# Kernel tuning notes

Measured on AMD Instinct MI355X. Metric: run time of the kernel, lower is better.

Reference implementation:

```python
import jax, jax.numpy as jnp
import numpy as np

VOCAB, EMBED, H = 32000, 128, 128
B, T = 32, 2048


def setup_inputs() -> dict:
    key = jax.random.key(0)
    ks = jax.random.split(key, 8)
    tokens = jax.random.randint(ks[0], (B, T), 0, VOCAB, dtype=jnp.int32)
    emb = jax.random.normal(ks[1], (VOCAB, EMBED), jnp.float32) * 0.05
    # layer 0: input EMBED -> H ; layer 1: H -> H
    Wx0 = jax.random.normal(ks[2], (EMBED, H), jnp.float32) * (1.0 / np.sqrt(EMBED))
    Wh0 = jax.random.normal(ks[3], (H, H), jnp.float32) * (1.0 / np.sqrt(H))
    b0 = jnp.zeros((H,), jnp.float32)
    Wx1 = jax.random.normal(ks[4], (H, H), jnp.float32) * (1.0 / np.sqrt(H))
    Wh1 = jax.random.normal(ks[5], (H, H), jnp.float32) * (1.0 / np.sqrt(H))
    b1 = jnp.zeros((H,), jnp.float32)
    return {"tokens": tokens, "emb": emb, "Wx0": Wx0, "Wh0": Wh0, "b0": b0,
            "Wx1": Wx1, "Wh1": Wh1, "b1": b1}


def _simple_rnn(x, mask, Wx, Wh, b):
    # x: [B,T,Din], mask: [B,T] bool. Keras masked-step semantics: at masked
    # steps, state (== output for SimpleRNN) carries over unchanged.
    xt = jnp.swapaxes(x, 0, 1)                 # [T,B,Din]
    xproj = xt @ Wx + b                        # precompute input projection [T,B,H]
    mt = jnp.swapaxes(mask, 0, 1)[..., None]   # [T,B,1]
    h0 = jnp.zeros((x.shape[0], Wh.shape[0]), x.dtype)

    def step(h, inp):
        xp, m = inp
        h_new = jnp.tanh(xp + h @ Wh)
        h = jnp.where(m, h_new, h)
        return h, h

    _, ys = jax.lax.scan(step, h0, (xproj, mt))
    return jnp.swapaxes(ys, 0, 1)              # [B,T,H]


def reference(tokens, emb, Wx0, Wh0, b0, Wx1, Wh1, b1):
    mask = tokens != 0                          # mask_zero=True
    x = emb[tokens]                             # [B,T,E]
    x = _simple_rnn(x, mask, Wx0, Wh0, b0)
    x = _simple_rnn(x, mask, Wx1, Wh1, b1)
    return x
```

## Files before the change

kernel.cpp:

```cpp
#include <hip/hip_runtime.h>
#include <math.h>

#define BB 32
#define TT 2048
#define HH 128

#define LDS_BARRIER() asm volatile("s_waitcnt lgkmcnt(0)\n\ts_barrier" ::: "memory")

#define QPERM_F(v, CTRL)                                                      \
  __int_as_float(__builtin_amdgcn_update_dpp(                                 \
      0, __float_as_int(v), (CTRL), 0xF, 0xF, true))

template <bool GATHER>
__global__ __launch_bounds__(256) void proj_kernel(
    const float* __restrict__ src, const int* __restrict__ tokens,
    const float* __restrict__ W, const float* __restrict__ bias,
    float* __restrict__ out) {
  const int tid = threadIdx.x;
  const int jj = tid & 31;
  const int rr = tid >> 5;
  const int base = blockIdx.x * 64;

  __shared__ __align__(16) float srow[64][HH];
  __shared__ int stok[64];

  if (GATHER) {
    if (tid < 64) stok[tid] = tokens[base + tid];
    __syncthreads();
  }

#pragma unroll
  for (int i = 0; i < 8; ++i) {
    int idx = tid + i * 256;
    int row = idx >> 5;
    int c4 = idx & 31;
    const float* s = GATHER ? (src + (size_t)stok[row] * HH)
                            : (src + (size_t)(base + row) * HH);
    *(float4*)&srow[row][c4 * 4] = *(const float4*)&s[c4 * 4];
  }
  __syncthreads();

  float4 b4 = *(const float4*)&bias[jj * 4];
  float4 acc[8];
#pragma unroll
  for (int i = 0; i < 8; ++i) acc[i] = b4;

  for (int k = 0; k < HH; ++k) {
    float4 w4 = *(const float4*)&W[k * HH + jj * 4];
#pragma unroll
    for (int i = 0; i < 8; ++i) {
      float e = srow[rr * 8 + i][k];
      acc[i].x += e * w4.x;
      acc[i].y += e * w4.y;
      acc[i].z += e * w4.z;
      acc[i].w += e * w4.w;
    }
  }

#pragma unroll
  for (int i = 0; i < 8; ++i) {
    int row = base + rr * 8 + i;
    *(float4*)&out[(size_t)row * HH + jj * 4] = acc[i];
  }
}

__global__ __launch_bounds__(512) void rnn_kernel(
    float* io, const float* __restrict__ Wh, const int* __restrict__ tokens) {
  const int b = blockIdx.x;
  const int tid = threadIdx.x;
  const int j = tid >> 2;
  const int p = tid & 3;
  const int lane = tid & 63;

  float w[32];
#pragma unroll
  for (int c = 0; c < 32; ++c) {
    int k = 16 * (c >> 2) + 4 * p + (c & 3);
    w[c] = Wh[k * HH + j];
  }

  const int* tok = tokens + b * TT;
  unsigned bits = 0;
#pragma unroll
  for (int i = 0; i < 8; ++i) {
    int4 tk = *(const int4*)&tok[lane * 32 + i * 4];
    bits |= (unsigned)(tk.x != 0) << (i * 4 + 0);
    bits |= (unsigned)(tk.y != 0) << (i * 4 + 1);
    bits |= (unsigned)(tk.z != 0) << (i * 4 + 2);
    bits |= (unsigned)(tk.w != 0) << (i * 4 + 3);
  }

  __shared__ __align__(16) float hs[2][HH];
  if (tid < HH) hs[0][tid] = 0.0f;

  float* xp = io + (size_t)b * TT * HH;

  float h = 0.0f;
  float xcur = xp[(size_t)p * HH + j];
  LDS_BARRIER();

#define RNN_STEP(Q)                                                           \
  {                                                                           \
    const int t = t0 + (Q);                                                   \
    const float* hb = hs[t & 1];                                              \
    float a0 = 0.f, a1 = 0.f, a2 = 0.f, a3 = 0.f;                             \
    _Pragma("unroll") for (int i = 0; i < 8; ++i) {                           \
      float4 hv = *(const float4*)&hb[16 * i + 4 * p];                        \
      a0 += hv.x * w[4 * i + 0];                                              \
      a1 += hv.y * w[4 * i + 1];                                              \
      a2 += hv.z * w[4 * i + 2];                                              \
      a3 += hv.w * w[4 * i + 3];                                              \
    }                                                                         \
    float acc = (a0 + a1) + (a2 + a3);                                        \
    acc += QPERM_F(acc, 0xB1);                                     \
    acc += QPERM_F(acc, 0x4E);                                     \
    float x = QPERM_F(xcur, (Q)*0x55);             \
    float s = acc + x;                                                        \
    unsigned word =                                                           \
        (unsigned)__builtin_amdgcn_readlane((int)bits, t >> 5);               \
    int m = (word >> (t & 31)) & 1;                                           \
    float ax = fabsf(s);                                                      \
    float e = __expf(-2.0f * ax);                                             \
    float th = (1.0f - e) * __builtin_amdgcn_rcpf(1.0f + e);                  \
    th = copysignf(th, s);                                                    \
    h = m ? th : h;                                                           \
    if (p == 0) {                                                             \
      xp[(size_t)t * HH + j] = h;                   \
      hs[(t + 1) & 1][j] = h;                                  \
    }                                                                         \
    LDS_BARRIER();                                                            \
  }

  for (int t0 = 0; t0 < TT; t0 += 4) {
    float xnext = 0.0f;
    if (t0 + 4 < TT) xnext = xp[(size_t)(t0 + 4 + p) * HH + j];
    RNN_STEP(0)
    RNN_STEP(1)
    RNN_STEP(2)
    RNN_STEP(3)
    xcur = xnext;
  }
#undef RNN_STEP
}

extern "C" void kernel_launch(void* const* d_in, const int* in_sizes, int n_in,
                              void* d_out, int out_size, void* d_ws,
                              size_t ws_size, hipStream_t stream) {
  const int* tokens = (const int*)d_in[0];
  const float* emb = (const float*)d_in[1];
  const float* Wx0 = (const float*)d_in[2];
  const float* Wh0 = (const float*)d_in[3];
  const float* b0 = (const float*)d_in[4];
  const float* Wx1 = (const float*)d_in[5];
  const float* Wh1 = (const float*)d_in[6];
  const float* b1 = (const float*)d_in[7];
  float* out = (float*)d_out;
  float* ws = (float*)d_ws;

  const int rows = BB * TT;
  const int proj_blocks = rows / 64;

  proj_kernel<true><<<proj_blocks, 256, 0, stream>>>(emb, tokens, Wx0, b0, ws);
  rnn_kernel<<<BB, 512, 0, stream>>>(ws, Wh0, tokens);
  proj_kernel<false><<<proj_blocks, 256, 0, stream>>>(ws, nullptr, Wx1, b1, out);
  rnn_kernel<<<BB, 512, 0, stream>>>(out, Wh1, tokens);
}
```

Baseline: 1.406 ms.

## Fuse both RNN layers into one wavefront-pipelined kernel

Runs the two RNN layers in a single 1024-thread block per batch row. Threads 0-511 run layer 0 and threads 512-1023 run layer 1 one step behind, reading layer 0's hidden state straight from shared memory. The layer-1 input projection is folded into the recurrence, which removes the second projection kernel, one launch and an HBM round trip of the intermediate sequence. In exchange each layer-1 step does twice the dot-product work, the two layers share barriers in lockstep, and the doubled thread count raises register pressure.

```diff
diff --git a/kernel.cpp b/kernel.cpp
--- a/kernel.cpp
+++ b/kernel.cpp
@@ -11,7 +11,6 @@
   __int_as_float(__builtin_amdgcn_update_dpp(                                 \
       0, __float_as_int(v), (CTRL), 0xF, 0xF, true))
 
-template <bool GATHER>
 __global__ __launch_bounds__(256) void proj_kernel(
     const float* __restrict__ src, const int* __restrict__ tokens,
     const float* __restrict__ W, const float* __restrict__ bias,
@@ -24,18 +23,15 @@
   __shared__ __align__(16) float srow[64][HH];
   __shared__ int stok[64];
 
-  if (GATHER) {
-    if (tid < 64) stok[tid] = tokens[base + tid];
-    __syncthreads();
-  }
+  if (tid < 64) stok[tid] = tokens[base + tid];
+  __syncthreads();
 
 #pragma unroll
   for (int i = 0; i < 8; ++i) {
     int idx = tid + i * 256;
     int row = idx >> 5;
     int c4 = idx & 31;
-    const float* s = GATHER ? (src + (size_t)stok[row] * HH)
-                            : (src + (size_t)(base + row) * HH);
+    const float* s = src + (size_t)stok[row] * HH;
     *(float4*)&srow[row][c4 * 4] = *(const float4*)&s[c4 * 4];
   }
   __syncthreads();
@@ -64,20 +60,18 @@
   }
 }
 
-__global__ __launch_bounds__(512) void rnn_kernel(
-    float* io, const float* __restrict__ Wh, const int* __restrict__ tokens) {
+__global__ __launch_bounds__(1024) void rnn_fused(
+    const float* __restrict__ xp0, float* __restrict__ out,
+    const float* __restrict__ Wh0, const float* __restrict__ Wx1,
+    const float* __restrict__ Wh1, const float* __restrict__ b1,
+    const int* __restrict__ tokens) {
   const int b = blockIdx.x;
   const int tid = threadIdx.x;
-  const int j = tid >> 2;
-  const int p = tid & 3;
+  const bool isL0 = (tid < 512);
+  const int sub = tid & 511;
+  const int j = sub >> 2;
+  const int p = sub & 3;
   const int lane = tid & 63;
-
-  float w[32];
-#pragma unroll
-  for (int c = 0; c < 32; ++c) {
-    int k = 16 * (c >> 2) + 4 * p + (c & 3);
-    w[c] = Wh[k * HH + j];
-  }
 
   const int* tok = tokens + b * TT;
   unsigned bits = 0;
@@ -90,57 +84,123 @@
     bits |= (unsigned)(tk.w != 0) << (i * 4 + 3);
   }
 
-  __shared__ __align__(16) float hs[2][HH];
-  if (tid < HH) hs[0][tid] = 0.0f;
-
-  float* xp = io + (size_t)b * TT * HH;
-
-  float h = 0.0f;
-  float xcur = xp[(size_t)p * HH + j];
+  __shared__ __align__(16) float hs0[2][HH];
+  __shared__ __align__(16) float hs1[2][HH];
+  if (tid < HH) {
+    hs0[0][tid] = 0.0f;
+    hs0[1][tid] = 0.0f;
+    hs1[0][tid] = 0.0f;
+    hs1[1][tid] = 0.0f;
+  }
   LDS_BARRIER();
 
-#define RNN_STEP(Q)                                                           \
+  if (isL0) {
+    float w0[32];
+#pragma unroll
+    for (int c = 0; c < 32; ++c) {
+      int k = 16 * (c >> 2) + 4 * p + (c & 3);
+      w0[c] = Wh0[k * HH + j];
+    }
+    const float* xb = xp0 + (size_t)b * TT * HH;
+    float h0 = 0.0f;
+    float xc = xb[(size_t)p * HH + j];
+
+#define L0_STEP(Q)                                                            \
   {                                                                           \
     const int t = t0 + (Q);                                                   \
-    const float* hb = hs[t & 1];                                              \
+    const float* hb = hs0[(Q) & 1];                                           \
     float a0 = 0.f, a1 = 0.f, a2 = 0.f, a3 = 0.f;                             \
     _Pragma("unroll") for (int i = 0; i < 8; ++i) {                           \
       float4 hv = *(const float4*)&hb[16 * i + 4 * p];                        \
-      a0 += hv.x * w[4 * i + 0];                                              \
-      a1 += hv.y * w[4 * i + 1];                                              \
-      a2 += hv.z * w[4 * i + 2];                                              \
-      a3 += hv.w * w[4 * i + 3];                                              \
+      a0 += hv.x * w0[4 * i + 0];                                             \
+      a1 += hv.y * w0[4 * i + 1];                                             \
+      a2 += hv.z * w0[4 * i + 2];                                             \
+      a3 += hv.w * w0[4 * i + 3];                                             \
     }                                                                         \
     float acc = (a0 + a1) + (a2 + a3);                                        \
-    acc += QPERM_F(acc, 0xB1);                                     \
-    acc += QPERM_F(acc, 0x4E);                                     \
-    float x = QPERM_F(xcur, (Q)*0x55);             \
-    float s = acc + x;                                                        \
-    unsigned word =                                                           \
-        (unsigned)__builtin_amdgcn_readlane((int)bits, t >> 5);               \
+    acc += QPERM_F(acc, 0xB1);                                                \
+    acc += QPERM_F(acc, 0x4E);                                                \
+    float sx = acc + QPERM_F(xc, (Q) * 0x55);                                 \
+    unsigned word = (unsigned)__builtin_amdgcn_readlane((int)bits, t >> 5);   \
     int m = (word >> (t & 31)) & 1;                                           \
-    float ax = fabsf(s);                                                      \
-    float e = __expf(-2.0f * ax);                                             \
-    float th = (1.0f - e) * __builtin_amdgcn_rcpf(1.0f + e);                  \
-    th = copysignf(th, s);                                                    \
-    h = m ? th : h;                                                           \
+    float e = __expf(-2.0f * fabsf(sx));                                      \
+    float th = copysignf((1.0f - e) * __builtin_amdgcn_rcpf(1.0f + e), sx);   \
+    h0 = m ? th : h0;                                                         \
+    if (p == 0) hs0[((Q) + 1) & 1][j] = h0;                                   \
+    LDS_BARRIER();                                                            \
+  }
+
+    for (int t0 = 0; t0 < TT; t0 += 4) {
+      float xn = 0.0f;
+      if (t0 + 4 < TT) xn = xb[(size_t)(t0 + 4 + p) * HH + j];
+      L0_STEP(0)
+      L0_STEP(1)
+      L0_STEP(2)
+      L0_STEP(3)
+      xc = xn;
+    }
+#undef L0_STEP
+  } else {
+    float wx[32], wh[32];
+#pragma unroll
+    for (int c = 0; c < 32; ++c) {
+      int k = 16 * (c >> 2) + 4 * p + (c & 3);
+      wx[c] = Wx1[k * HH + j];
+      wh[c] = Wh1[k * HH + j];
+    }
+    const float bias1 = b1[j];
+    float* ob = out + (size_t)b * TT * HH;
+    float h1 = 0.0f;
+
+#define L1_BODY(PH, PAR)                                                      \
+  {                                                                           \
+    const int t = (PH)-1;                                                     \
+    const float* yb = hs0[(PAR)];                                             \
+    const float* hb = hs1[(PAR)];                                             \
+    float a0 = 0.f, a1 = 0.f, a2 = 0.f, a3 = 0.f;                             \
+    float c0 = 0.f, c1 = 0.f, c2 = 0.f, c3 = 0.f;                             \
+    _Pragma("unroll") for (int i = 0; i < 8; ++i) {                           \
+      float4 yv = *(const float4*)&yb[16 * i + 4 * p];                        \
+      float4 hv = *(const float4*)&hb[16 * i + 4 * p];                        \
+      a0 += yv.x * wx[4 * i + 0];                                             \
+      a1 += yv.y * wx[4 * i + 1];                                             \
+      a2 += yv.z * wx[4 * i + 2];                                             \
+      a3 += yv.w * wx[4 * i + 3];                                             \
+      c0 += hv.x * wh[4 * i + 0];                                             \
+      c1 += hv.y * wh[4 * i + 1];                                             \
+      c2 += hv.z * wh[4 * i + 2];                                             \
+      c3 += hv.w * wh[4 * i + 3];                                             \
+    }                                                                         \
+    float acc = ((a0 + a1) + (a2 + a3)) + ((c0 + c1) + (c2 + c3));            \
+    acc += QPERM_F(acc, 0xB1);                                                \
+    acc += QPERM_F(acc, 0x4E);                                                \
+    float sx = acc + bias1;                                                   \
+    unsigned word = (unsigned)__builtin_amdgcn_readlane((int)bits, t >> 5);   \
+    int m = (word >> (t & 31)) & 1;                                           \
+    float e = __expf(-2.0f * fabsf(sx));                                      \
+    float th = copysignf((1.0f - e) * __builtin_amdgcn_rcpf(1.0f + e), sx);   \
+    h1 = m ? th : h1;                                                         \
     if (p == 0) {                                                             \
-      xp[(size_t)t * HH + j] = h;                   \
-      hs[(t + 1) & 1][j] = h;                                  \
+      ob[(size_t)t * HH + j] = h1;                                            \
+      hs1[(PAR) ^ 1][j] = h1;                                                 \
     }                                                                         \
-    LDS_BARRIER();                                                            \
-  }
-
-  for (int t0 = 0; t0 < TT; t0 += 4) {
-    float xnext = 0.0f;
-    if (t0 + 4 < TT) xnext = xp[(size_t)(t0 + 4 + p) * HH + j];
-    RNN_STEP(0)
-    RNN_STEP(1)
-    RNN_STEP(2)
-    RNN_STEP(3)
-    xcur = xnext;
-  }
-#undef RNN_STEP
+  }
+
+    for (int ph0 = 0; ph0 < TT; ph0 += 4) {
+      if (ph0 > 0) {
+        L1_BODY(ph0 + 0, 0)
+      }
+      LDS_BARRIER();
+      L1_BODY(ph0 + 1, 1)
+      LDS_BARRIER();
+      L1_BODY(ph0 + 2, 0)
+      LDS_BARRIER();
+      L1_BODY(ph0 + 3, 1)
+      LDS_BARRIER();
+    }
+    L1_BODY(TT, 0)
+#undef L1_BODY
+  }
 }
 
 extern "C" void kernel_launch(void* const* d_in, const int* in_sizes, int n_in,
@@ -160,8 +220,6 @@
   const int rows = BB * TT;
   const int proj_blocks = rows / 64;
 
-  proj_kernel<true><<<proj_blocks, 256, 0, stream>>>(emb, tokens, Wx0, b0, ws);
-  rnn_kernel<<<BB, 512, 0, stream>>>(ws, Wh0, tokens);
-  proj_kernel<false><<<proj_blocks, 256, 0, stream>>>(ws, nullptr, Wx1, b1, out);
-  rnn_kernel<<<BB, 512, 0, stream>>>(out, Wh1, tokens);
+  proj_kernel<<<proj_blocks, 256, 0, stream>>>(emb, tokens, Wx0, b0, ws);
+  rnn_fused<<<BB, 1024, 0, stream>>>(ws, out, Wh0, Wx1, Wh1, b1, tokens);
 }
```

Measured after the change: 4.575 ms. +225.3%, slower.

## Remap RNN recurrence to 8 lanes per two output columns

Applied to the files above, without the earlier changes.

Reorganizes the recurrent matvec so each group of 8 lanes computes two hidden columns (cp and cp+64), each lane covering 16 k-values per column, with a three-stage DPP reduction within the 8-lane group. The input projection values are now loaded per lane into registers for four steps rather than broadcast via DPP. The goal is to halve the LDS reads of h per column and shorten the per-step dependency chain, at the cost of an extra DPP reduction stage, more per-lane global loads and two writer lanes per group.

```diff
diff --git a/kernel.cpp b/kernel.cpp
--- a/kernel.cpp
+++ b/kernel.cpp
@@ -7,7 +7,7 @@
 
 #define LDS_BARRIER() asm volatile("s_waitcnt lgkmcnt(0)\n\ts_barrier" ::: "memory")
 
-#define QPERM_F(v, CTRL)                                                      \
+#define DPP_F(v, CTRL)                                                        \
   __int_as_float(__builtin_amdgcn_update_dpp(                                 \
       0, __float_as_int(v), (CTRL), 0xF, 0xF, true))
 
@@ -68,15 +68,17 @@
     float* io, const float* __restrict__ Wh, const int* __restrict__ tokens) {
   const int b = blockIdx.x;
   const int tid = threadIdx.x;
-  const int j = tid >> 2;
-  const int p = tid & 3;
+  const int cp = tid >> 3;
+  const int p = tid & 7;
   const int lane = tid & 63;
+  const int colsel = cp + ((p & 1) << 6);
 
-  float w[32];
+  float w0[16], w1[16];
 #pragma unroll
-  for (int c = 0; c < 32; ++c) {
-    int k = 16 * (c >> 2) + 4 * p + (c & 3);
-    w[c] = Wh[k * HH + j];
+  for (int c = 0; c < 16; ++c) {
+    int k = 32 * (c >> 2) + 4 * p + (c & 3);
+    w0[c] = Wh[k * HH + cp];
+    w1[c] = Wh[k * HH + cp + 64];
   }
 
   const int* tok = tokens + b * TT;
@@ -95,50 +97,68 @@
 
   float* xp = io + (size_t)b * TT * HH;
 
+  float xr[4];
+#pragma unroll
+  for (int i = 0; i < 4; ++i) xr[i] = xp[(size_t)i * HH + colsel];
+
   float h = 0.0f;
-  float xcur = xp[(size_t)p * HH + j];
   LDS_BARRIER();
 
 #define RNN_STEP(Q)                                                           \
   {                                                                           \
     const int t = t0 + (Q);                                                   \
-    const float* hb = hs[t & 1];                                              \
+    const float* hb = hs[(Q) & 1];                                            \
     float a0 = 0.f, a1 = 0.f, a2 = 0.f, a3 = 0.f;                             \
-    _Pragma("unroll") for (int i = 0; i < 8; ++i) {                           \
-      float4 hv = *(const float4*)&hb[16 * i + 4 * p];                        \
-      a0 += hv.x * w[4 * i + 0];                                              \
-      a1 += hv.y * w[4 * i + 1];                                              \
-      a2 += hv.z * w[4 * i + 2];                                              \
-      a3 += hv.w * w[4 * i + 3];                                              \
+    float c0 = 0.f, c1 = 0.f, c2 = 0.f, c3 = 0.f;                             \
+    _Pragma("unroll") for (int i = 0; i < 4; ++i) {                           \
+      float4 hv = *(const float4*)&hb[32 * i + 4 * p];                        \
+      a0 += hv.x * w0[4 * i + 0];                                             \
+      a1 += hv.y * w0[4 * i + 1];                                             \
+      a2 += hv.z * w0[4 * i + 2];                                             \
+      a3 += hv.w * w0[4 * i + 3];                                             \
+      c0 += hv.x * w1[4 * i + 0];                                             \
+      c1 += hv.y * w1[4 * i + 1];                                             \
+      c2 += hv.z * w1[4 * i + 2];                                             \
+      c3 += hv.w * w1[4 * i + 3];                                             \
     }                                                                         \
-    float acc = (a0 + a1) + (a2 + a3);                                        \
-    acc += QPERM_F(acc, 0xB1);                                     \
-    acc += QPERM_F(acc, 0x4E);                                     \
-    float x = QPERM_F(xcur, (Q)*0x55);             \
-    float s = acc + x;                                                        \
-    unsigned word =                                                           \
-        (unsigned)__builtin_amdgcn_readlane((int)bits, t >> 5);               \
+    float accA = (a0 + a1) + (a2 + a3);                                       \
+    float accB = (c0 + c1) + (c2 + c3);                                       \
+    accA += DPP_F(accA, 0xB1);                           \
+    accB += DPP_F(accB, 0xB1);                                                \
+    accA += DPP_F(accA, 0x4E);                           \
+    accB += DPP_F(accB, 0x4E);                                                \
+    accA += DPP_F(accA, 0x141);                \
+    accB += DPP_F(accB, 0x141);                                               \
+    float acc = (p & 1) ? accB : accA;                                        \
+    float sx = acc + xr[(Q)];                                                 \
+    unsigned word = (unsigned)__builtin_amdgcn_readlane((int)bits, t >> 5);   \
     int m = (word >> (t & 31)) & 1;                                           \
-    float ax = fabsf(s);                                                      \
-    float e = __expf(-2.0f * ax);                                             \
-    float th = (1.0f - e) * __builtin_amdgcn_rcpf(1.0f + e);                  \
-    th = copysignf(th, s);                                                    \
+    float e = __expf(-2.0f * fabsf(sx));                                      \
+    float th = copysignf((1.0f - e) * __builtin_amdgcn_rcpf(1.0f + e), sx);   \
     h = m ? th : h;                                                           \
-    if (p == 0) {                                                             \
-      xp[(size_t)t * HH + j] = h;                   \
-      hs[(t + 1) & 1][j] = h;                                  \
+    if (p < 2) {                                                              \
+      xp[(size_t)t * HH + colsel] = h;              \
+      hs[((Q) + 1) & 1][colsel] = h;                           \
     }                                                                         \
     LDS_BARRIER();                                                            \
   }
 
   for (int t0 = 0; t0 < TT; t0 += 4) {
-    float xnext = 0.0f;
-    if (t0 + 4 < TT) xnext = xp[(size_t)(t0 + 4 + p) * HH + j];
+    float xn0 = 0.f, xn1 = 0.f, xn2 = 0.f, xn3 = 0.f;
+    if (t0 + 4 < TT) {
+      xn0 = xp[(size_t)(t0 + 4) * HH + colsel];
+      xn1 = xp[(size_t)(t0 + 5) * HH + colsel];
+      xn2 = xp[(size_t)(t0 + 6) * HH + colsel];
+      xn3 = xp[(size_t)(t0 + 7) * HH + colsel];
+    }
     RNN_STEP(0)
     RNN_STEP(1)
     RNN_STEP(2)
     RNN_STEP(3)
-    xcur = xnext;
+    xr[0] = xn0;
+    xr[1] = xn1;
+    xr[2] = xn2;
+    xr[3] = xn3;
   }
 #undef RNN_STEP
 }
```

Result: slower. 1.493 ms (+6.2%).

## Pipeline both RNN layers concurrently with chunked flag handoff and fused layer-1 projection

Applied to the files above, without the earlier changes.

Replaces the sequential layer-0 RNN, layer-1 projection and layer-1 RNN launches with one kernel of 64 blocks. The first 32 blocks run layer 0 and publish progress per 64-step chunk through global release flags. The other 32 run layer 1, spinning on those flags and computing the Wx1 input projection inline from a register ring buffer. This overlaps the two serial recurrences and removes the separate projection pass, at the cost of a doubled per-step dot product in layer 1 and cross-block spin-waiting that assumes all 64 blocks are co-resident. The old path remains as a fallback when the workspace is too small.

```diff
diff --git a/kernel.cpp b/kernel.cpp
--- a/kernel.cpp
+++ b/kernel.cpp
@@ -4,6 +4,9 @@
 #define BB 32
 #define TT 2048
 #define HH 128
+#define CHUNK 64
+#define NCH (TT / CHUNK)
+#define WS_HDR 4096
 
 #define LDS_BARRIER() asm volatile("s_waitcnt lgkmcnt(0)\n\ts_barrier" ::: "memory")
 
@@ -15,11 +18,14 @@
 __global__ __launch_bounds__(256) void proj_kernel(
     const float* __restrict__ src, const int* __restrict__ tokens,
     const float* __restrict__ W, const float* __restrict__ bias,
-    float* __restrict__ out) {
+    float* __restrict__ out, int* flags) {
   const int tid = threadIdx.x;
   const int jj = tid & 31;
   const int rr = tid >> 5;
   const int base = blockIdx.x * 64;
+
+  if (GATHER && flags != nullptr && blockIdx.x == 0 && tid < BB)
+    flags[tid] = 0;
 
   __shared__ __align__(16) float srow[64][HH];
   __shared__ int stok[64];
@@ -94,15 +100,14 @@
   if (tid < HH) hs[0][tid] = 0.0f;
 
   float* xp = io + (size_t)b * TT * HH;
-
   float h = 0.0f;
-  float xcur = xp[(size_t)p * HH + j];
+  float xc = xp[(size_t)p * HH + j];
   LDS_BARRIER();
 
 #define RNN_STEP(Q)                                                           \
   {                                                                           \
     const int t = t0 + (Q);                                                   \
-    const float* hb = hs[t & 1];                                              \
+    const float* hb = hs[(Q) & 1];                                            \
     float a0 = 0.f, a1 = 0.f, a2 = 0.f, a3 = 0.f;                             \
     _Pragma("unroll") for (int i = 0; i < 8; ++i) {                           \
       float4 hv = *(const float4*)&hb[16 * i + 4 * p];                        \
@@ -112,35 +117,191 @@
       a3 += hv.w * w[4 * i + 3];                                              \
     }                                                                         \
     float acc = (a0 + a1) + (a2 + a3);                                        \
-    acc += QPERM_F(acc, 0xB1);                                     \
-    acc += QPERM_F(acc, 0x4E);                                     \
-    float x = QPERM_F(xcur, (Q)*0x55);             \
-    float s = acc + x;                                                        \
-    unsigned word =                                                           \
-        (unsigned)__builtin_amdgcn_readlane((int)bits, t >> 5);               \
+    acc += QPERM_F(acc, 0xB1);                                                \
+    acc += QPERM_F(acc, 0x4E);                                                \
+    float sx = acc + QPERM_F(xc, (Q) * 0x55);                                 \
+    unsigned word = (unsigned)__builtin_amdgcn_readlane((int)bits, t >> 5);   \
     int m = (word >> (t & 31)) & 1;                                           \
-    float ax = fabsf(s);                                                      \
-    float e = __expf(-2.0f * ax);                                             \
-    float th = (1.0f - e) * __builtin_amdgcn_rcpf(1.0f + e);                  \
-    th = copysignf(th, s);                                                    \
+    float e = __expf(-2.0f * fabsf(sx));                                      \
+    float th = copysignf((1.0f - e) * __builtin_amdgcn_rcpf(1.0f + e), sx);   \
     h = m ? th : h;                                                           \
     if (p == 0) {                                                             \
-      xp[(size_t)t * HH + j] = h;                   \
-      hs[(t + 1) & 1][j] = h;                                  \
+      xp[(size_t)t * HH + j] = h;                                             \
+      hs[((Q) + 1) & 1][j] = h;                                               \
     }                                                                         \
     LDS_BARRIER();                                                            \
   }
 
   for (int t0 = 0; t0 < TT; t0 += 4) {
-    float xnext = 0.0f;
-    if (t0 + 4 < TT) xnext = xp[(size_t)(t0 + 4 + p) * HH + j];
+    float xn = 0.0f;
+    if (t0 + 4 < TT) xn = xp[(size_t)(t0 + 4 + p) * HH + j];
     RNN_STEP(0)
     RNN_STEP(1)
     RNN_STEP(2)
     RNN_STEP(3)
-    xcur = xnext;
+    xc = xn;
   }
 #undef RNN_STEP
+}
+
+__global__ __launch_bounds__(512) void rnn_pipe(
+    float* y0buf, float* __restrict__ out, const float* __restrict__ Wh0,
+    const float* __restrict__ Wx1, const float* __restrict__ Wh1,
+    const float* __restrict__ b1, const int* __restrict__ tokens,
+    int* flags) {
+  const int blk = blockIdx.x;
+  const bool isL0 = (blk < BB);
+  const int b = isL0 ? blk : blk - BB;
+  const int tid = threadIdx.x;
+  const int j = tid >> 2;
+  const int p = tid & 3;
+  const int lane = tid & 63;
+
+  const int* tok = tokens + b * TT;
+  unsigned bits = 0;
+#pragma unroll
+  for (int i = 0; i < 8; ++i) {
+    int4 tk = *(const int4*)&tok[lane * 32 + i * 4];
+    bits |= (unsigned)(tk.x != 0) << (i * 4 + 0);
+    bits |= (unsigned)(tk.y != 0) << (i * 4 + 1);
+    bits |= (unsigned)(tk.z != 0) << (i * 4 + 2);
+    bits |= (unsigned)(tk.w != 0) << (i * 4 + 3);
+  }
+
+  __shared__ __align__(16) float hs[2][HH];
+  if (tid < HH) hs[0][tid] = 0.0f;
+
+  float* y0 = y0buf + (size_t)b * TT * HH;
+
+  if (isL0) {
+    float w[32];
+#pragma unroll
+    for (int c = 0; c < 32; ++c) {
+      int k = 16 * (c >> 2) + 4 * p + (c & 3);
+      w[c] = Wh0[k * HH + j];
+    }
+    float h = 0.0f;
+    float xc = y0[(size_t)p * HH + j];
+    LDS_BARRIER();
+
+#define L0_STEP(Q)                                                            \
+  {                                                                           \
+    const int t = t0 + (Q);                                                   \
+    const float* hb = hs[(Q) & 1];                                            \
+    float a0 = 0.f, a1 = 0.f, a2 = 0.f, a3 = 0.f;                             \
+    _Pragma("unroll") for (int i = 0; i < 8; ++i) {                           \
+      float4 hv = *(const float4*)&hb[16 * i + 4 * p];                        \
+      a0 += hv.x * w[4 * i + 0];                                              \
+      a1 += hv.y * w[4 * i + 1];                                              \
+      a2 += hv.z * w[4 * i + 2];                                              \
+      a3 += hv.w * w[4 * i + 3];                                              \
+    }                                                                         \
+    float acc = (a0 + a1) + (a2 + a3);                                        \
+    acc += QPERM_F(acc, 0xB1);                                                \
+    acc += QPERM_F(acc, 0x4E);                                                \
+    float sx = acc + QPERM_F(xc, (Q) * 0x55);                                 \
+    unsigned word = (unsigned)__builtin_amdgcn_readlane((int)bits, t >> 5);   \
+    int m = (word >> (t & 31)) & 1;                                           \
+    float e = __expf(-2.0f * fabsf(sx));                                      \
+    float th = copysignf((1.0f - e) * __builtin_amdgcn_rcpf(1.0f + e), sx);   \
+    h = m ? th : h;                                                           \
+    if (p == 0) {                                                             \
+      y0[(size_t)t * HH + j] = h;                                             \
+      hs[((Q) + 1) & 1][j] = h;                                               \
+    }                                                                         \
+    LDS_BARRIER();                                                            \
+  }
+
+    for (int c = 0; c < NCH; ++c) {
+      for (int t0 = c * CHUNK; t0 < (c + 1) * CHUNK; t0 += 4) {
+        float xn = 0.0f;
+        if (t0 + 4 < TT) xn = y0[(size_t)(t0 + 4 + p) * HH + j];
+        L0_STEP(0)
+        L0_STEP(1)
+        L0_STEP(2)
+        L0_STEP(3)
+        xc = xn;
+      }
+      asm volatile("s_waitcnt vmcnt(0)" ::: "memory");
+      __syncthreads();
+      if (tid == 0) {
+        __threadfence();
+        __hip_atomic_store(&flags[b], c + 1, __ATOMIC_RELEASE,
+                           __HIP_MEMORY_SCOPE_AGENT);
+      }
+    }
+#undef L0_STEP
+  } else {
+    float wx[32], wh[32];
+#pragma unroll
+    for (int c = 0; c < 32; ++c) {
+      int k = 16 * (c >> 2) + 4 * p + (c & 3);
+      wx[c] = Wx1[k * HH + j];
+      wh[c] = Wh1[k * HH + j];
+    }
+    const float bias1 = b1[j];
+    float* ob = out + (size_t)b * TT * HH;
+    float h = 0.0f;
+    float4 ring0[8], ring1[8];
+    LDS_BARRIER();
+
+#define L1_STEP(Q, RG, RGN)                                                   \
+  {                                                                           \
+    const int t = t0 + (Q);                                                   \
+    const float* hb = hs[(Q) & 1];                                            \
+    float a0 = 0.f, a1 = 0.f, a2 = 0.f, a3 = 0.f;                             \
+    _Pragma("unroll") for (int i = 0; i < 8; ++i) {                           \
+      float4 hv = *(const float4*)&hb[16 * i + 4 * p];                        \
+      float4 yv = RG[i];                                                      \
+      a0 += hv.x * wh[4 * i + 0] + yv.x * wx[4 * i + 0];                      \
+      a1 += hv.y * wh[4 * i + 1] + yv.y * wx[4 * i + 1];                      \
+      a2 += hv.z * wh[4 * i + 2] + yv.z * wx[4 * i + 2];                      \
+      a3 += hv.w * wh[4 * i + 3] + yv.w * wx[4 * i + 3];                      \
+    }                                                                         \
+    if (t + 2 < TT) {                                                         \
+      const float* nsrc = y0 + (size_t)(t + 2) * HH + 4 * p;                  \
+      _Pragma("unroll") for (int i = 0; i < 8; ++i)                           \
+          RGN[i] = *(const float4*)(nsrc + 16 * i);                           \
+    }                                                                         \
+    float acc = (a0 + a1) + (a2 + a3);                                        \
+    acc += QPERM_F(acc, 0xB1);                                                \
+    acc += QPERM_F(acc, 0x4E);                                                \
+    float sx = acc + bias1;                                                   \
+    unsigned word = (unsigned)__builtin_amdgcn_readlane((int)bits, t >> 5);   \
+    int m = (word >> (t & 31)) & 1;                                           \
+    float e = __expf(-2.0f * fabsf(sx));                                      \
+    float th = copysignf((1.0f - e) * __builtin_amdgcn_rcpf(1.0f + e), sx);   \
+    h = m ? th : h;                                                           \
+    if (p == 0) {                                                             \
+      ob[(size_t)t * HH + j] = h;                                             \
+      hs[((Q) + 1) & 1][j] = h;                                               \
+    }                                                                         \
+    LDS_BARRIER();                                                            \
+  }
+
+    for (int c = 0; c < NCH; ++c) {
+      const int need = (c + 2 > NCH) ? NCH : (c + 2);
+      while (__hip_atomic_load(&flags[b], __ATOMIC_ACQUIRE,
+                               __HIP_MEMORY_SCOPE_AGENT) < need)
+        __builtin_amdgcn_s_sleep(8);
+      if (c == 0) {
+        const float* s0 = y0 + 4 * p;
+        const float* s1 = y0 + HH + 4 * p;
+#pragma unroll
+        for (int i = 0; i < 8; ++i) {
+          ring0[i] = *(const float4*)(s0 + 16 * i);
+          ring1[i] = *(const float4*)(s1 + 16 * i);
+        }
+      }
+      for (int t0 = c * CHUNK; t0 < (c + 1) * CHUNK; t0 += 4) {
+        L1_STEP(0, ring0, ring0)
+        L1_STEP(1, ring1, ring1)
+        L1_STEP(2, ring0, ring0)
+        L1_STEP(3, ring1, ring1)
+      }
+    }
+#undef L1_STEP
+  }
 }
 
 extern "C" void kernel_launch(void* const* d_in, const int* in_sizes, int n_in,
@@ -155,13 +316,25 @@
   const float* Wh1 = (const float*)d_in[6];
   const float* b1 = (const float*)d_in[7];
   float* out = (float*)d_out;
-  float* ws = (float*)d_ws;
-
+
+  const size_t buf_bytes = (size_t)BB * TT * HH * sizeof(float);
   const int rows = BB * TT;
   const int proj_blocks = rows / 64;
 
-  proj_kernel<true><<<proj_blocks, 256, 0, stream>>>(emb, tokens, Wx0, b0, ws);
-  rnn_kernel<<<BB, 512, 0, stream>>>(ws, Wh0, tokens);
-  proj_kernel<false><<<proj_blocks, 256, 0, stream>>>(ws, nullptr, Wx1, b1, out);
-  rnn_kernel<<<BB, 512, 0, stream>>>(out, Wh1, tokens);
+  if (ws_size >= buf_bytes + WS_HDR) {
+    int* flags = (int*)d_ws;
+    float* buf = (float*)((char*)d_ws + WS_HDR);
+    proj_kernel<true><<<proj_blocks, 256, 0, stream>>>(emb, tokens, Wx0, b0,
+                                                       buf, flags);
+    rnn_pipe<<<2 * BB, 512, 0, stream>>>(buf, out, Wh0, Wx1, Wh1, b1, tokens,
+                                         flags);
+  } else {
+    float* ws = (float*)d_ws;
+    proj_kernel<true><<<proj_blocks, 256, 0, stream>>>(emb, tokens, Wx0, b0,
+                                                       ws, nullptr);
+    rnn_kernel<<<BB, 512, 0, stream>>>(ws, Wh0, tokens);
+    proj_kernel<false><<<proj_blocks, 256, 0, stream>>>(ws, nullptr, Wx1, b1,
+                                                        out, nullptr);
+    rnn_kernel<<<BB, 512, 0, stream>>>(out, Wh1, tokens);
+  }
 }
```

After: 1.684 ms. 1.2x slower.
